# Kernel optimization log

Measured on AMD Instinct MI355X. Metric: run time of the kernel, lower is better.

The kernel has to match this reference:

```python
import jax, jax.numpy as jnp
import numpy as np

B, N, D = 256, 64, 512        # batch, num_patches, dim
H, DH = 8, 64                 # heads, dim_head
INNER = H * DH                # 512
SCALE = DH ** -0.5


def setup_inputs() -> dict:
    key = jax.random.key(0)
    k0, k1, k2, k3, k4 = jax.random.split(key, 5)
    s = 0.02
    return {
        "x": jax.random.normal(k0, (B, N, D), jnp.float32),
        "Wq": jax.random.normal(k1, (D, INNER), jnp.float32) * s,      # to_q (no bias)
        "Wkv": jax.random.normal(k2, (D, 2 * INNER), jnp.float32) * s,  # to_k_v (no bias)
        "Wout": jax.random.normal(k3, (INNER, D), jnp.float32) * s,     # to_out Linear weight
        "bout": jnp.zeros((D,), jnp.float32),                           # to_out Linear bias
        "Wspec": jax.random.normal(k4, (N, 3 * N), jnp.float32) * s,    # to_qkv_spec (no bias)
    }


def reference(x, Wq, Wkv, Wout, bout, Wspec):
    b, n, d = x.shape
    # --- center-token spatial attention ---
    median_idx = n // 2
    x_center = jnp.broadcast_to(x[:, median_idx:median_idx + 1, :], (b, n, d))
    q = (x_center @ Wq).reshape(b, n, H, DH).transpose(0, 2, 1, 3)   # b h n dh
    kv = x @ Wkv                                                      # b n 2*inner
    k, v = jnp.split(kv, 2, axis=-1)
    k = k.reshape(b, n, H, DH).transpose(0, 2, 1, 3)                  # b h n dh
    v = v.reshape(b, n, H, DH).transpose(0, 2, 1, 3)                  # b h n dh
    attn = jax.nn.softmax(jnp.einsum('bhnd,bhmd->bhnm', q, k) * SCALE, axis=-1)
    out = jnp.einsum('bhnm,bhmd->bhnd', attn, v)                      # b h n dh
    out = out.transpose(0, 2, 1, 3).reshape(b, n, INNER)              # b n inner
    spatial_out = out @ Wout + bout                                   # b n d (dropout=0 -> identity)
    # --- transposed spectral attention ---
    x_t = x.transpose(0, 2, 1)                                        # b d n
    qkv = x_t @ Wspec                                                 # b d 3n
    q_s, k_s, _v_s = jnp.split(qkv, 3, axis=-1)                       # v_spec is unused in the original
    spec_weights = jax.nn.softmax(
        jnp.einsum('bdn,ben->bde', q_s, k_s) * SCALE, axis=-1)        # b d d
    # --- final combining matmul ---
    return jnp.einsum('bnd,bde->bne', spatial_out, spec_weights)      # b n d
```

## Files before the change

### kernel.cpp

```cpp
#include <hip/hip_runtime.h>

#define NP 64
#define DIM 512
#define NH 8
#define SCALE 0.125f

typedef __attribute__((ext_vector_type(4))) float f32x4;
typedef __attribute__((ext_vector_type(8))) short bf16x8;

#define WS_C   0
#define WS_MT  8192
#define WS_PT  4202496
#define WS_U   8396800
#define WS_Y   10493952

static __device__ __forceinline__ unsigned short f2bf(float f) {
  unsigned int u = __builtin_bit_cast(unsigned int, f);
  u += 0x7fffu + ((u >> 16) & 1u);
  return (unsigned short)(u >> 16);
}
static __device__ __forceinline__ float bf2f(unsigned short s) {
  return __builtin_bit_cast(float, ((unsigned int)s) << 16);
}
static __device__ __forceinline__ unsigned pk2(float a, float b) {
  return (unsigned)f2bf(a) | ((unsigned)f2bf(b) << 16);
}

__global__ __launch_bounds__(512)
void kw_prep(const float* __restrict__ Wq, const float* __restrict__ Wkv,
             const float* __restrict__ Wout, const float* __restrict__ Wspec,
             char* __restrict__ ws) {
  __shared__ float wa[64 * 65];
  __shared__ float wb[64 * 65];
  const int t = threadIdx.x;
  const int blk = blockIdx.x;
  const int sr = t >> 3, sc8 = (t & 7) * 8;

  if (blk == 1024) {
    #pragma unroll
    for (int cc = 0; cc < 8; ++cc) {
      wa[sr * 65 + sc8 + cc] = Wspec[sr * 192 + sc8 + cc];
      wb[sr * 65 + sc8 + cc] = Wspec[sr * 192 + 64 + sc8 + cc];
    }
    __syncthreads();
    const int m = sr, mm0 = sc8;
    float acc[8] = {0.f, 0.f, 0.f, 0.f, 0.f, 0.f, 0.f, 0.f};
    for (int n = 0; n < 64; ++n) {
      float qv = wa[m * 65 + n];
      #pragma unroll
      for (int j = 0; j < 8; ++j)
        acc[j] = fmaf(qv, wb[(mm0 + j) * 65 + n], acc[j]);
    }
    uint4 pk;
    pk.x = pk2(acc[0] * SCALE, acc[1] * SCALE);
    pk.y = pk2(acc[2] * SCALE, acc[3] * SCALE);
    pk.z = pk2(acc[4] * SCALE, acc[5] * SCALE);
    pk.w = pk2(acc[6] * SCALE, acc[7] * SCALE);
    *(uint4*)(ws + WS_C + m * 128 + ((mm0 * 2) ^ ((m & 7) << 4))) = pk;
    return;
  }

  const bool isP = blk >= 512;
  const int id = blk & 511;
  const int h = id >> 6, et = (id >> 3) & 7, dt = id & 7;

  const float* sa = isP ? (Wkv + (size_t)(dt * 64 + sr) * 1024 + 512 + h * 64)
                        : (Wq + (size_t)(dt * 64 + sr) * 512 + h * 64);
  const float* sb = isP ? (Wout + (size_t)(h * 64 + sr) * 512 + et * 64)
                        : (Wkv + (size_t)(et * 64 + sr) * 1024 + h * 64);
  {
    float4 a0 = *(const float4*)(sa + sc8), a1 = *(const float4*)(sa + sc8 + 4);
    float* d = wa + sr * 65 + sc8;
    d[0] = a0.x; d[1] = a0.y; d[2] = a0.z; d[3] = a0.w;
    d[4] = a1.x; d[5] = a1.y; d[6] = a1.z; d[7] = a1.w;
    float4 b0 = *(const float4*)(sb + sc8), b1 = *(const float4*)(sb + sc8 + 4);
    float* e = wb + sr * 65 + sc8;
    e[0] = b0.x; e[1] = b0.y; e[2] = b0.z; e[3] = b0.w;
    e[4] = b1.x; e[5] = b1.y; e[6] = b1.z; e[7] = b1.w;
  }
  __syncthreads();

  const int er = sr, dc8 = sc8;
  float acc[8] = {0.f, 0.f, 0.f, 0.f, 0.f, 0.f, 0.f, 0.f};
  if (!isP) {
    for (int j = 0; j < 64; ++j) {
      float bv = wb[er * 65 + j];
      #pragma unroll
      for (int dd = 0; dd < 8; ++dd)
        acc[dd] = fmaf(bv, wa[(dc8 + dd) * 65 + j], acc[dd]);
    }
  } else {
    for (int j = 0; j < 64; ++j) {
      float bv = wb[j * 65 + er];
      #pragma unroll
      for (int dd = 0; dd < 8; ++dd)
        acc[dd] = fmaf(bv, wa[(dc8 + dd) * 65 + j], acc[dd]);
    }
  }
  uint4 pk;
  pk.x = pk2(acc[0], acc[1]);
  pk.y = pk2(acc[2], acc[3]);
  pk.z = pk2(acc[4], acc[5]);
  pk.w = pk2(acc[6], acc[7]);
  if (!isP)
    *(uint4*)(ws + WS_MT + ((size_t)(h * 512 + et * 64 + er) * 512 + dt * 64 + dc8) * 2) = pk;
  else
    *(uint4*)(ws + WS_PT + ((size_t)(et * 64 + er) * 4096 + h * 512 + dt * 64 + dc8) * 2) = pk;
}

#define GEMM_LDS 131072
__global__ __launch_bounds__(512, 2)
void ku_u(const float* __restrict__ x, const char* __restrict__ ws,
          char* __restrict__ ws_u) {
  extern __shared__ char sm[];
  char* At = sm;
  char* Bt = sm + 65536;
  const int t = threadIdx.x, lane = t & 63, wave = t >> 6;
  const int bt = blockIdx.x >> 6, nt = blockIdx.x & 63;
  const int b0 = bt * 64, n0 = nt * 64;
  const char* Mt = ws + WS_MT;

  #pragma unroll
  for (int i = 0; i < 8; ++i) {
    const int r = wave * 8 + i;
    const float4* xr = (const float4*)(x + ((size_t)(b0 + r) * 64 + 32) * 512);
    float4 a = xr[lane], c = xr[64 + lane];
    uint2 pa = {pk2(a.x, a.y), pk2(a.z, a.w)};
    uint2 pc = {pk2(c.x, c.y), pk2(c.z, c.w)};
    const int swz = (r & 7) << 4;
    const int byt = (8 * (lane & 15)) ^ swz;
    *(uint2*)(At + (lane >> 4) * 8192 + r * 128 + byt) = pa;
    *(uint2*)(At + (4 + (lane >> 4)) * 8192 + r * 128 + byt) = pc;
  }
  #pragma unroll
  for (int i = 0; i < 8; ++i) {
    const int r = wave * 8 + i;
    uint4 v = ((const uint4*)(Mt + (size_t)(n0 + r) * 1024))[lane];
    *(uint4*)(Bt + (lane >> 3) * 8192 + r * 128 + ((16 * (lane & 7)) ^ ((r & 7) << 4))) = v;
  }
  __syncthreads();

  const int lo = ((lane & 15) * 128) + (((lane >> 4) * 16) ^ ((lane & 7) << 4));
  const int hi = ((lane & 15) * 128) + ((((lane >> 4) * 16) + 64) ^ ((lane & 7) << 4));
  const int bsub = wave & 3, npair = wave >> 2;

  f32x4 c0 = {0.f, 0.f, 0.f, 0.f}, c1 = {0.f, 0.f, 0.f, 0.f};
  #pragma unroll
  for (int kc = 0; kc < 8; ++kc) {
    const char* ab = At + kc * 8192 + bsub * 2048;
    bf16x8 aL = *(const bf16x8*)(ab + lo);
    bf16x8 aH = *(const bf16x8*)(ab + hi);
    const char* bb0 = Bt + kc * 8192 + (npair * 2) * 2048;
    const char* bb1 = bb0 + 2048;
    c0 = __builtin_amdgcn_mfma_f32_16x16x32_bf16(aL, *(const bf16x8*)(bb0 + lo), c0, 0, 0, 0);
    c0 = __builtin_amdgcn_mfma_f32_16x16x32_bf16(aH, *(const bf16x8*)(bb0 + hi), c0, 0, 0, 0);
    c1 = __builtin_amdgcn_mfma_f32_16x16x32_bf16(aL, *(const bf16x8*)(bb1 + lo), c1, 0, 0, 0);
    c1 = __builtin_amdgcn_mfma_f32_16x16x32_bf16(aH, *(const bf16x8*)(bb1 + hi), c1, 0, 0, 0);
  }
  unsigned short* U = (unsigned short*)ws_u;
  const int brow = b0 + bsub * 16 + (lane >> 4) * 4;
  const int nc0 = n0 + (npair * 2) * 16 + (lane & 15);
  #pragma unroll
  for (int r = 0; r < 4; ++r) {
    U[(size_t)(brow + r) * 4096 + nc0] = f2bf(c0[r]);
    U[(size_t)(brow + r) * 4096 + nc0 + 16] = f2bf(c1[r]);
  }
}

__global__ __launch_bounds__(512)
void k2_attn(const float* __restrict__ x, const char* __restrict__ ws_u,
             char* __restrict__ ws_y) {
  __shared__ float ul[8 * 512];
  __shared__ float scoreL[8 * 64];
  __shared__ float pT[64 * 8];
  const int t = threadIdx.x;
  const int lane = t & 63;
  const int wave = t >> 6;
  const int b = blockIdx.x;
  const float* xb = x + (size_t)b * NP * DIM;

  {
    uint4 v = ((const uint4*)(ws_u + (size_t)b * 8192))[t];
    const unsigned short* pv = (const unsigned short*)&v;
    float* d = ul + t * 8;
    #pragma unroll
    for (int g = 0; g < 8; ++g) d[g] = bf2f(pv[g]);
  }
  __syncthreads();

  {
    float4 uf0[8], uf1[8];
    #pragma unroll
    for (int h = 0; h < 8; ++h) {
      uf0[h] = *(const float4*)(ul + h * 512 + 4 * lane);
      uf1[h] = *(const float4*)(ul + h * 512 + 256 + 4 * lane);
    }
    #pragma unroll 2
    for (int i = 0; i < 8; ++i) {
      const int m = wave * 8 + i;
      const float4* xr = (const float4*)(xb + (size_t)m * DIM);
      float4 xv0 = xr[lane];
      float4 xv1 = xr[64 + lane];
      #pragma unroll
      for (int h = 0; h < 8; ++h) {
        float p = xv0.x * uf0[h].x + xv0.y * uf0[h].y + xv0.z * uf0[h].z + xv0.w * uf0[h].w
                + xv1.x * uf1[h].x + xv1.y * uf1[h].y + xv1.z * uf1[h].z + xv1.w * uf1[h].w;
        p += __shfl_xor(p, 1);
        p += __shfl_xor(p, 2);
        p += __shfl_xor(p, 4);
        p += __shfl_xor(p, 8);
        p += __shfl_xor(p, 16);
        p += __shfl_xor(p, 32);
        if (lane == 0) scoreL[h * 64 + m] = p;
      }
    }
  }
  __syncthreads();

  {
    float sc = scoreL[wave * 64 + lane] * SCALE;
    float mx = sc;
    #pragma unroll
    for (int off = 32; off > 0; off >>= 1)
      mx = fmaxf(mx, __shfl_xor(mx, off));
    float ev = __expf(sc - mx);
    float sm = ev;
    #pragma unroll
    for (int off = 32; off > 0; off >>= 1)
      sm += __shfl_xor(sm, off);
    pT[lane * NH + wave] = ev / sm;
  }
  __syncthreads();

  {
    float acc[NH];
    #pragma unroll
    for (int h = 0; h < NH; ++h) acc[h] = 0.f;
    #pragma unroll 2
    for (int m = 0; m < NP; ++m) {
      float xv = xb[(size_t)m * DIM + t];
      const float4* pp = (const float4*)(pT + m * NH);
      float4 p0 = pp[0], p1 = pp[1];
      acc[0] = fmaf(p0.x, xv, acc[0]);
      acc[1] = fmaf(p0.y, xv, acc[1]);
      acc[2] = fmaf(p0.z, xv, acc[2]);
      acc[3] = fmaf(p0.w, xv, acc[3]);
      acc[4] = fmaf(p1.x, xv, acc[4]);
      acc[5] = fmaf(p1.y, xv, acc[5]);
      acc[6] = fmaf(p1.z, xv, acc[6]);
      acc[7] = fmaf(p1.w, xv, acc[7]);
    }
    unsigned short* Y = (unsigned short*)ws_y;
    #pragma unroll
    for (int h = 0; h < NH; ++h)
      Y[(size_t)b * 4096 + h * 512 + t] = f2bf(acc[h]);
  }
}

__global__ __launch_bounds__(512, 2)
void ks_s(const char* __restrict__ ws_y, const char* __restrict__ ws_pt,
          float* __restrict__ Spart) {
  extern __shared__ char sm[];
  char* At = sm;
  char* Bt = sm + 65536;
  const int t = threadIdx.x, lane = t & 63, wave = t >> 6;
  const int bt = blockIdx.x >> 6, et = (blockIdx.x >> 3) & 7, sl = blockIdx.x & 7;
  const int b0 = bt * 64, e0 = et * 64;
  const size_t kb2 = (size_t)sl * 1024;

  #pragma unroll
  for (int i = 0; i < 8; ++i) {
    const int r = wave * 8 + i;
    const int byt = (16 * (lane & 7)) ^ ((r & 7) << 4);
    uint4 va = ((const uint4*)(ws_y + (size_t)(b0 + r) * 8192 + kb2))[lane];
    *(uint4*)(At + (lane >> 3) * 8192 + r * 128 + byt) = va;
    uint4 vb = ((const uint4*)(ws_pt + (size_t)(e0 + r) * 8192 + kb2))[lane];
    *(uint4*)(Bt + (lane >> 3) * 8192 + r * 128 + byt) = vb;
  }
  __syncthreads();

  const int lo = ((lane & 15) * 128) + (((lane >> 4) * 16) ^ ((lane & 7) << 4));
  const int hi = ((lane & 15) * 128) + ((((lane >> 4) * 16) + 64) ^ ((lane & 7) << 4));
  const int bsub = wave & 3, epair = wave >> 2;

  f32x4 c0 = {0.f, 0.f, 0.f, 0.f}, c1 = {0.f, 0.f, 0.f, 0.f};
  #pragma unroll
  for (int kc = 0; kc < 8; ++kc) {
    const char* ab = At + kc * 8192 + bsub * 2048;
    bf16x8 aL = *(const bf16x8*)(ab + lo);
    bf16x8 aH = *(const bf16x8*)(ab + hi);
    const char* bb0 = Bt + kc * 8192 + (epair * 2) * 2048;
    const char* bb1 = bb0 + 2048;
    c0 = __builtin_amdgcn_mfma_f32_16x16x32_bf16(aL, *(const bf16x8*)(bb0 + lo), c0, 0, 0, 0);
    c0 = __builtin_amdgcn_mfma_f32_16x16x32_bf16(aH, *(const bf16x8*)(bb0 + hi), c0, 0, 0, 0);
    c1 = __builtin_amdgcn_mfma_f32_16x16x32_bf16(aL, *(const bf16x8*)(bb1 + lo), c1, 0, 0, 0);
    c1 = __builtin_amdgcn_mfma_f32_16x16x32_bf16(aH, *(const bf16x8*)(bb1 + hi), c1, 0, 0, 0);
  }
  const int brow = b0 + bsub * 16 + (lane >> 4) * 4;
  const int ec0 = e0 + (epair * 2) * 16 + (lane & 15);
  #pragma unroll
  for (int r = 0; r < 4; ++r) {
    Spart[((size_t)sl * 256 + brow + r) * 512 + ec0] = c0[r];
    Spart[((size_t)sl * 256 + brow + r) * 512 + ec0 + 16] = c1[r];
  }
}

#define K4_LDS 75776
__global__ __launch_bounds__(1024)
void k4_spec(const float* __restrict__ x, const char* __restrict__ Cws,
             const float* __restrict__ Spart, const float* __restrict__ bout,
             float* __restrict__ out) {
  extern __shared__ char smem[];
  char* region0 = smem;
  char* Cc = smem + 65536;
  float* s_l = (float*)(smem + 73728);

  const int t = threadIdx.x;
  const int lane = t & 63;
  const int wave = t >> 6;
  const int b = blockIdx.x;
  const float* xb = x + (size_t)b * NP * DIM;

  const int lo_off = ((lane & 15) * 128) + ((((lane >> 4) * 16)) ^ ((lane & 7) << 4));
  const int hi_off = ((lane & 15) * 128) + ((((lane >> 4) * 16) + 64) ^ ((lane & 7) << 4));

  {
    const int d = t & 511;
    const int cbase = (t >> 9) * 4;
    #pragma unroll
    for (int ci = 0; ci < 4; ++ci) {
      const int c = cbase + ci;
      float v0 = xb[(c * 8 + 0) * DIM + d];
      float v1 = xb[(c * 8 + 1) * DIM + d];
      float v2 = xb[(c * 8 + 2) * DIM + d];
      float v3 = xb[(c * 8 + 3) * DIM + d];
      float v4 = xb[(c * 8 + 4) * DIM + d];
      float v5 = xb[(c * 8 + 5) * DIM + d];
      float v6 = xb[(c * 8 + 6) * DIM + d];
      float v7 = xb[(c * 8 + 7) * DIM + d];
      uint4 pk;
      pk.x = pk2(v0, v1);
      pk.y = pk2(v2, v3);
      pk.z = pk2(v4, v5);
      pk.w = pk2(v6, v7);
      *(uint4*)(region0 + d * 128 + ((c * 16) ^ ((d & 7) << 4))) = pk;
    }
    if (t < 512) {
      ((uint4*)Cc)[t] = ((const uint4*)Cws)[t];
      float sacc = bout[t];
      #pragma unroll
      for (int sl = 0; sl < 8; ++sl)
        sacc += Spart[((size_t)sl * 256 + b) * 512 + t];
      s_l[t] = sacc;
    }
  }
  __syncthreads();

  bf16x8 pa0[2], pa1[2];
  #pragma unroll
  for (int pass = 0; pass < 2; ++pass) {
    const int d0 = pass * 256 + wave * 16;
    pa0[pass] = *(const bf16x8*)(region0 + d0 * 128 + lo_off);
    pa1[pass] = *(const bf16x8*)(region0 + d0 * 128 + hi_off);
  }

  uint2 pkW2[2][4];
  {
    bf16x8 af0[4], af1[4];
    #pragma unroll
    for (int mt = 0; mt < 4; ++mt) {
      af0[mt] = *(const bf16x8*)(Cc + mt * 16 * 128 + lo_off);
      af1[mt] = *(const bf16x8*)(Cc + mt * 16 * 128 + hi_off);
    }
    #pragma unroll
    for (int etl = 0; etl < 2; ++etl) {
      const int e0 = (wave * 2 + etl) * 16;
      bf16x8 b0 = *(const bf16x8*)(region0 + e0 * 128 + lo_off);
      bf16x8 b1 = *(const bf16x8*)(region0 + e0 * 128 + hi_off);
      #pragma unroll
      for (int mt = 0; mt < 4; ++mt) {
        f32x4 c = {0.f, 0.f, 0.f, 0.f};
        c = __builtin_amdgcn_mfma_f32_16x16x32_bf16(af0[mt], b0, c, 0, 0, 0);
        c = __builtin_amdgcn_mfma_f32_16x16x32_bf16(af1[mt], b1, c, 0, 0, 0);
        pkW2[etl][mt].x = pk2(c[0], c[1]);
        pkW2[etl][mt].y = pk2(c[2], c[3]);
      }
    }
  }
  __syncthreads();

  {
    #pragma unroll
    for (int etl = 0; etl < 2; ++etl) {
      const int e = (wave * 2 + etl) * 16 + (lane & 15);
      #pragma unroll
      for (int mt = 0; mt < 4; ++mt) {
        const int mrow = mt * 16 + (lane >> 4) * 4;
        *(uint2*)(region0 + e * 128 + ((mrow * 2) ^ ((e & 7) << 4))) = pkW2[etl][mt];
      }
    }
  }
  __syncthreads();

  float treg[32];
  #pragma unroll
  for (int et = 0; et < 32; ++et) treg[et] = 0.f;

  #pragma unroll
  for (int pass = 0; pass < 2; ++pass) {
    const int d0 = pass * 256 + wave * 16;
    bf16x8 a0 = pa0[pass];
    bf16x8 a1 = pa1[pass];

    float rs[4] = {0.f, 0.f, 0.f, 0.f};
    #pragma unroll 4
    for (int et = 0; et < 32; ++et) {
      bf16x8 b0 = *(const bf16x8*)(region0 + et * 2048 + lo_off);
      bf16x8 b1 = *(const bf16x8*)(region0 + et * 2048 + hi_off);
      f32x4 c = {0.f, 0.f, 0.f, 0.f};
      c = __builtin_amdgcn_mfma_f32_16x16x32_bf16(a0, b0, c, 0, 0, 0);
      c = __builtin_amdgcn_mfma_f32_16x16x32_bf16(a1, b1, c, 0, 0, 0);
      rs[0] += __expf(c[0]);
      rs[1] += __expf(c[1]);
      rs[2] += __expf(c[2]);
      rs[3] += __expf(c[3]);
    }
    #pragma unroll
    for (int r = 0; r < 4; ++r) {
      rs[r] += __shfl_xor(rs[r], 1);
      rs[r] += __shfl_xor(rs[r], 2);
      rs[r] += __shfl_xor(rs[r], 4);
      rs[r] += __shfl_xor(rs[r], 8);
    }
    float coef[4];
    #pragma unroll
    for (int r = 0; r < 4; ++r)
      coef[r] = s_l[d0 + (lane >> 4) * 4 + r] / rs[r];

    #pragma unroll 4
    for (int et = 0; et < 32; ++et) {
      bf16x8 b0 = *(const bf16x8*)(region0 + et * 2048 + lo_off);
      bf16x8 b1 = *(const bf16x8*)(region0 + et * 2048 + hi_off);
      f32x4 c = {0.f, 0.f, 0.f, 0.f};
      c = __builtin_amdgcn_mfma_f32_16x16x32_bf16(a0, b0, c, 0, 0, 0);
      c = __builtin_amdgcn_mfma_f32_16x16x32_bf16(a1, b1, c, 0, 0, 0);
      float tp = treg[et];
      tp = fmaf(coef[0], __expf(c[0]), tp);
      tp = fmaf(coef[1], __expf(c[1]), tp);
      tp = fmaf(coef[2], __expf(c[2]), tp);
      tp = fmaf(coef[3], __expf(c[3]), tp);
      treg[et] = tp;
    }
  }
  __syncthreads();

  #pragma unroll
  for (int et = 0; et < 32; ++et) {
    treg[et] += __shfl_xor(treg[et], 16);
    treg[et] += __shfl_xor(treg[et], 32);
  }
  float* wpart = (float*)region0;
  if (lane < 16) {
    #pragma unroll
    for (int et = 0; et < 32; ++et)
      wpart[wave * 512 + et * 16 + lane] = treg[et];
  }
  __syncthreads();

  const int e = t & 511;
  float tf = 0.f;
  #pragma unroll
  for (int w = 0; w < 16; ++w) tf += wpart[w * 512 + e];

  const int n0 = (t >> 9) * 32;
  float* ob = out + (size_t)b * NP * DIM + e;
  #pragma unroll 4
  for (int n = n0; n < n0 + 32; ++n) ob[n * DIM] = tf;
}

extern "C" void kernel_launch(void* const* d_in, const int* in_sizes, int n_in,
                              void* d_out, int out_size, void* d_ws, size_t ws_size,
                              hipStream_t stream) {
  (void)in_sizes; (void)n_in; (void)out_size; (void)ws_size;
  const float* x     = (const float*)d_in[0];
  const float* Wq    = (const float*)d_in[1];
  const float* Wkv   = (const float*)d_in[2];
  const float* Wout  = (const float*)d_in[3];
  const float* bout  = (const float*)d_in[4];
  const float* Wspec = (const float*)d_in[5];
  float* out = (float*)d_out;

  char* ws = (char*)d_ws;

  hipFuncSetAttribute(reinterpret_cast<const void*>(ku_u),
                      hipFuncAttributeMaxDynamicSharedMemorySize, GEMM_LDS);
  hipFuncSetAttribute(reinterpret_cast<const void*>(ks_s),
                      hipFuncAttributeMaxDynamicSharedMemorySize, GEMM_LDS);
  hipFuncSetAttribute(reinterpret_cast<const void*>(k4_spec),
                      hipFuncAttributeMaxDynamicSharedMemorySize, K4_LDS);

  kw_prep<<<dim3(1025), dim3(512), 0, stream>>>(Wq, Wkv, Wout, Wspec, ws);
  ku_u   <<<dim3(256),  dim3(512), GEMM_LDS, stream>>>(x, ws, ws + WS_U);
  k2_attn<<<dim3(256),  dim3(512), 0, stream>>>(x, ws + WS_U, ws + WS_Y);
  ks_s   <<<dim3(256),  dim3(512), GEMM_LDS, stream>>>(ws + WS_Y, ws + WS_PT,
                                                       (float*)(ws + WS_MT));
  k4_spec<<<dim3(256),  dim3(1024), K4_LDS, stream>>>(x, ws, (const float*)(ws + WS_MT),
                                                      bout, out);
}
```

Baseline: 112.0 us.

## Cache exponentials in registers to avoid recomputing spectral score MFMAs

The spectral softmax stage previously ran its MFMA score computation twice per row block: once to get row sums and once to accumulate the weighted output. Now each wave covers half the e-tiles for four d-passes. It keeps the exponentials packed as bf16 in registers and combines partial row sums across wave pairs through a small LDS buffer with a barrier per pass. This removes the second MFMA and exp pass, but adds bf16 rounding of the exponentials, extra barriers and more register pressure.

```diff
diff --git a/kernel.cpp b/kernel.cpp
--- a/kernel.cpp
+++ b/kernel.cpp
@@ -305,7 +305,7 @@
   }
 }
 
-#define K4_LDS 75776
+#define K4_LDS 77824
 __global__ __launch_bounds__(1024)
 void k4_spec(const float* __restrict__ x, const char* __restrict__ Cws,
              const float* __restrict__ Spart, const float* __restrict__ bout,
@@ -314,6 +314,7 @@
   char* region0 = smem;
   char* Cc = smem + 65536;
   float* s_l = (float*)(smem + 73728);
+  float* rsx = (float*)(smem + 75776);
 
   const int t = threadIdx.x;
   const int lane = t & 63;
@@ -356,10 +357,10 @@
   }
   __syncthreads();
 
-  bf16x8 pa0[2], pa1[2];
-  #pragma unroll
-  for (int pass = 0; pass < 2; ++pass) {
-    const int d0 = pass * 256 + wave * 16;
+  bf16x8 pa0[4], pa1[4];
+  #pragma unroll
+  for (int pass = 0; pass < 4; ++pass) {
+    const int d0 = (pass * 8 + (wave & 7)) * 16;
     pa0[pass] = *(const bf16x8*)(region0 + d0 * 128 + lo_off);
     pa1[pass] = *(const bf16x8*)(region0 + d0 * 128 + hi_off);
   }
@@ -402,28 +403,36 @@
   }
   __syncthreads();
 
-  float treg[32];
-  #pragma unroll
-  for (int et = 0; et < 32; ++et) treg[et] = 0.f;
-
-  #pragma unroll
-  for (int pass = 0; pass < 2; ++pass) {
-    const int d0 = pass * 256 + wave * 16;
+  float treg[16];
+  #pragma unroll
+  for (int i = 0; i < 16; ++i) treg[i] = 0.f;
+  const int etbase = (wave >> 3) * 16;
+  const int rowg = (lane >> 4) * 4;
+
+  #pragma unroll
+  for (int pass = 0; pass < 4; ++pass) {
+    const int d0 = (pass * 8 + (wave & 7)) * 16;
     bf16x8 a0 = pa0[pass];
     bf16x8 a1 = pa1[pass];
 
     float rs[4] = {0.f, 0.f, 0.f, 0.f};
-    #pragma unroll 4
-    for (int et = 0; et < 32; ++et) {
+    uint2 pex[16];
+    #pragma unroll
+    for (int i = 0; i < 16; ++i) {
+      const int et = etbase + i;
       bf16x8 b0 = *(const bf16x8*)(region0 + et * 2048 + lo_off);
       bf16x8 b1 = *(const bf16x8*)(region0 + et * 2048 + hi_off);
       f32x4 c = {0.f, 0.f, 0.f, 0.f};
       c = __builtin_amdgcn_mfma_f32_16x16x32_bf16(a0, b0, c, 0, 0, 0);
       c = __builtin_amdgcn_mfma_f32_16x16x32_bf16(a1, b1, c, 0, 0, 0);
-      rs[0] += __expf(c[0]);
-      rs[1] += __expf(c[1]);
-      rs[2] += __expf(c[2]);
-      rs[3] += __expf(c[3]);
+      uint2 p;
+      p.x = pk2(__expf(c[0]), __expf(c[1]));
+      p.y = pk2(__expf(c[2]), __expf(c[3]));
+      pex[i] = p;
+      rs[0] += bf2f((unsigned short)(p.x & 0xffffu));
+      rs[1] += bf2f((unsigned short)(p.x >> 16));
+      rs[2] += bf2f((unsigned short)(p.y & 0xffffu));
+      rs[3] += bf2f((unsigned short)(p.y >> 16));
     }
     #pragma unroll
     for (int r = 0; r < 4; ++r) {
@@ -432,45 +441,49 @@
       rs[r] += __shfl_xor(rs[r], 4);
       rs[r] += __shfl_xor(rs[r], 8);
     }
+    const int pb = pass & 1;
+    if ((lane & 15) == 0) {
+      #pragma unroll
+      for (int r = 0; r < 4; ++r)
+        rsx[pb * 256 + wave * 16 + rowg + r] = rs[r];
+    }
+    __syncthreads();
     float coef[4];
     #pragma unroll
-    for (int r = 0; r < 4; ++r)
-      coef[r] = s_l[d0 + (lane >> 4) * 4 + r] / rs[r];
-
-    #pragma unroll 4
-    for (int et = 0; et < 32; ++et) {
-      bf16x8 b0 = *(const bf16x8*)(region0 + et * 2048 + lo_off);
-      bf16x8 b1 = *(const bf16x8*)(region0 + et * 2048 + hi_off);
-      f32x4 c = {0.f, 0.f, 0.f, 0.f};
-      c = __builtin_amdgcn_mfma_f32_16x16x32_bf16(a0, b0, c, 0, 0, 0);
-      c = __builtin_amdgcn_mfma_f32_16x16x32_bf16(a1, b1, c, 0, 0, 0);
-      float tp = treg[et];
-      tp = fmaf(coef[0], __expf(c[0]), tp);
-      tp = fmaf(coef[1], __expf(c[1]), tp);
-      tp = fmaf(coef[2], __expf(c[2]), tp);
-      tp = fmaf(coef[3], __expf(c[3]), tp);
-      treg[et] = tp;
-    }
-  }
-  __syncthreads();
-
-  #pragma unroll
-  for (int et = 0; et < 32; ++et) {
-    treg[et] += __shfl_xor(treg[et], 16);
-    treg[et] += __shfl_xor(treg[et], 32);
+    for (int r = 0; r < 4; ++r) {
+      const float rfull = rsx[pb * 256 + wave * 16 + rowg + r]
+                        + rsx[pb * 256 + (wave ^ 8) * 16 + rowg + r];
+      coef[r] = s_l[d0 + rowg + r] / rfull;
+    }
+    #pragma unroll
+    for (int i = 0; i < 16; ++i) {
+      uint2 p = pex[i];
+      float tp = treg[i];
+      tp = fmaf(coef[0], bf2f((unsigned short)(p.x & 0xffffu)), tp);
+      tp = fmaf(coef[1], bf2f((unsigned short)(p.x >> 16)), tp);
+      tp = fmaf(coef[2], bf2f((unsigned short)(p.y & 0xffffu)), tp);
+      tp = fmaf(coef[3], bf2f((unsigned short)(p.y >> 16)), tp);
+      treg[i] = tp;
+    }
+  }
+
+  #pragma unroll
+  for (int i = 0; i < 16; ++i) {
+    treg[i] += __shfl_xor(treg[i], 16);
+    treg[i] += __shfl_xor(treg[i], 32);
   }
   float* wpart = (float*)region0;
   if (lane < 16) {
     #pragma unroll
-    for (int et = 0; et < 32; ++et)
-      wpart[wave * 512 + et * 16 + lane] = treg[et];
+    for (int i = 0; i < 16; ++i)
+      wpart[(wave & 7) * 512 + (wave >> 3) * 256 + i * 16 + lane] = treg[i];
   }
   __syncthreads();
 
   const int e = t & 511;
   float tf = 0.f;
   #pragma unroll
-  for (int w = 0; w < 16; ++w) tf += wpart[w * 512 + e];
+  for (int w = 0; w < 8; ++w) tf += wpart[w * 512 + e];
 
   const int n0 = (t >> 9) * 32;
   float* ob = out + (size_t)b * NP * DIM + e;
```

New measurement: 240.1 us. +114.5%, slower.
